# Kernel optimization log

Measured on AMD Instinct MI355X. Metric: run time of the kernel, lower is better.

Reference implementation:

```python
import jax, jax.numpy as jnp
import numpy as np

N_MB = 4  # number of micro-behavior buckets; C = N_MB**2 + 1

def setup_inputs() -> dict:
    key = jax.random.key(0)
    k_q, k_k, k_b, k_w, k_a = jax.random.split(key, 5)
    b, h, S, d = 8, 8, 512, 64
    C = N_MB * N_MB + 1
    return {
        "query": jax.random.normal(k_q, (b, h, S, d), dtype=jnp.float32),
        "key": jax.random.normal(k_k, (b, h, S, d), dtype=jnp.float32),
        "b_seq": jax.random.randint(k_b, (b, S), 0, N_MB + 1, dtype=jnp.int32),
        "W1": jax.random.normal(k_w, (N_MB, h, d, d), dtype=jnp.float32) * 0.02,
        "alpha1": jax.random.normal(k_a, (C, N_MB, h), dtype=jnp.float32) * 0.02,
    }

def reference(query, key, b_seq, W1, alpha1):
    # bucket-pair index per (i, j) token pair; 0 if either token is padding
    bi = b_seq[:, :, None]  # [b, S, 1]
    bj = b_seq[:, None, :]  # [b, 1, S]
    b_mat = ((bi - 1) * N_MB + bj) * (bi * bj != 0).astype(jnp.int32)  # [b, S, S]
    # mix the n_mb base bilinear weights into C per-bucket-pair matrices
    W1_ = jnp.einsum('Bhmn,CBh->Chmn', W1, jax.nn.softmax(alpha1, axis=1))
    # full bilinear score for every bucket-pair class C (the wasteful part)
    att_all = jnp.einsum('bhim,Chmn,bhjn->bhijC', query, W1_, key)  # [b,h,S,S,C]
    # select the score matching each pair's bucket index
    idx = b_mat[:, None, :, :, None].astype(jnp.int32)  # [b,1,S,S,1] -> broadcast over h
    idx = jnp.broadcast_to(idx, att_all.shape[:4] + (1,))
    scores = jnp.take_along_axis(att_all, idx, axis=4)[..., 0]  # [b,h,S,S]
    return scores
```

## Files before the change

### kernel.cpp

```cpp
#include <hip/hip_runtime.h>
#include <stdint.h>

#define NB 4
#define NC 17
#define HH 8
#define SS 512
#define DD 64
#define CT 64

typedef __attribute__((ext_vector_type(8))) short bf16x8;
typedef __attribute__((ext_vector_type(4))) float f32x4;

#define WS_W1   0
#define WS_RIDX 1114112
#define WS_GST  (WS_RIDX + 16384)

__device__ __forceinline__ unsigned short f2bf(float f) {
  unsigned int x; __builtin_memcpy(&x, &f, 4);
  return (unsigned short)((x + 0x7fff + ((x >> 16) & 1)) >> 16);
}
__device__ __forceinline__ bf16x8 cvt8(float4 a, float4 b) {
  union { bf16x8 v; unsigned short u[8]; } t;
  t.u[0] = f2bf(a.x); t.u[1] = f2bf(a.y); t.u[2] = f2bf(a.z); t.u[3] = f2bf(a.w);
  t.u[4] = f2bf(b.x); t.u[5] = f2bf(b.y); t.u[6] = f2bf(b.z); t.u[7] = f2bf(b.w);
  return t.v;
}

__global__ __launch_bounds__(256) void k_prep(const int* __restrict__ bseq,
                                              const float* __restrict__ W1,
                                              const float* __restrict__ alpha,
                                              int* __restrict__ ridx,
                                              int* __restrict__ gst,
                                              unsigned short* __restrict__ W1mbf) {
  int tid = threadIdx.x;
  if (blockIdx.x < 8) {
    int b = blockIdx.x;
    __shared__ int cnt[5], base[6], cur[5];
    if (tid < 5) cnt[tid] = 0;
    __syncthreads();
    for (int j = tid; j < SS; j += blockDim.x) atomicAdd(&cnt[bseq[b * SS + j]], 1);
    __syncthreads();
    if (tid == 0) {
      base[0] = 0;
      for (int k = 0; k < 5; k++) base[k + 1] = base[k] + cnt[k];
      for (int k = 0; k < 6; k++) gst[b * 6 + k] = base[k];
    }
    __syncthreads();
    if (tid < 5) cur[tid] = base[tid];
    __syncthreads();
    for (int j = tid; j < SS; j += blockDim.x) {
      int p = atomicAdd(&cur[bseq[b * SS + j]], 1);
      ridx[b * SS + p] = j;
    }
  } else {
    int cb = blockIdx.x - 8;
    int c = cb >> 3, hh = cb & 7;
    __shared__ float sm[NB];
    if (tid == 0) {
      float a[NB], mx = -1e30f;
      for (int B = 0; B < NB; B++) { a[B] = alpha[(c * NB + B) * HH + hh]; mx = fmaxf(mx, a[B]); }
      float s = 0.f;
      for (int B = 0; B < NB; B++) { a[B] = __expf(a[B] - mx); s += a[B]; }
      for (int B = 0; B < NB; B++) sm[B] = a[B] / s;
    }
    __syncthreads();
    float s0 = sm[0], s1 = sm[1], s2 = sm[2], s3 = sm[3];
    const float* w0p = &W1[((0 * HH + hh) << 12)];
    const float* w1p = &W1[((1 * HH + hh) << 12)];
    const float* w2p = &W1[((2 * HH + hh) << 12)];
    const float* w3p = &W1[((3 * HH + hh) << 12)];
    unsigned short* dst = &W1mbf[((size_t)(c * HH + hh)) << 12];
    for (int idx = tid * 4; idx < DD * DD; idx += 1024) {
      float4 w0 = *(const float4*)(w0p + idx);
      float4 w1 = *(const float4*)(w1p + idx);
      float4 w2 = *(const float4*)(w2p + idx);
      float4 w3 = *(const float4*)(w3p + idx);
      union { unsigned short u[4]; uint2 v; } o;
      o.u[0] = f2bf(w0.x * s0 + w1.x * s1 + w2.x * s2 + w3.x * s3);
      o.u[1] = f2bf(w0.y * s0 + w1.y * s1 + w2.y * s2 + w3.y * s3);
      o.u[2] = f2bf(w0.z * s0 + w1.z * s1 + w2.z * s2 + w3.z * s3);
      o.u[3] = f2bf(w0.w * s0 + w1.w * s1 + w2.w * s2 + w3.w * s3);
      *(uint2*)(dst + idx) = o.v;
    }
  }
}

__global__ __launch_bounds__(768, 6) void k_fused(const float* __restrict__ query,
                                                  const float* __restrict__ key,
                                                  const int* __restrict__ bseq,
                                                  const unsigned short* __restrict__ W1mbf,
                                                  const int* __restrict__ ridx,
                                                  const int* __restrict__ gst,
                                                  float* __restrict__ out) {
  int bx = blockIdx.x;
  int bh = bx & 63, jt = bx >> 6;
  int b = bh >> 3, h = bh & 7;
  int j0 = jt * CT;
  int tid = threadIdx.x, wave = tid >> 6, lane = tid & 63;
  int quad = lane >> 4, l16 = lane & 15;

  __shared__ __align__(16) unsigned short Tl[5][CT][72];
  __shared__ int ord[CT];
  __shared__ int ridxs[SS];
  __shared__ int p1list[40], p2list[40];
  __shared__ int n1tot, n2tot;

  if (tid < SS) ridxs[tid] = ridx[b * SS + tid];

  if (wave == 0) {
    int mybj = bseq[b * SS + j0 + lane];
    unsigned long long mm[5];
    int pb[6];
    pb[0] = 0;
#pragma unroll
    for (int a = 0; a < 5; a++) {
      mm[a] = __ballot(mybj == a);
      pb[a + 1] = pb[a] + (int)__popcll(mm[a]);
    }
    int pos = pb[mybj] + (int)__popcll(mm[mybj] & ((1ull << lane) - 1ull));
    ord[pos] = lane;

    int n1b_[5]; int t = 0;
#pragma unroll
    for (int a = 0; a < 5; a++) {
      n1b_[a] = t;
      t += ((pb[a + 1] - pb[a] + 15) >> 4) * ((a == 0) ? 1 : 5);
    }
    if (lane == 0) n1tot = t;

    if (lane < 5) {
      int a = lane;
      int ls = pb[a], le = pb[a + 1];
      int w = n1b_[a];
      for (int t0 = ls; t0 < le; t0 += 16) {
        if (a == 0) {
          p1list[w++] = t0 | (le << 6) | (1 << 21);
        } else {
#pragma unroll
          for (int B = 0; B < 5; B++) {
            int c = (B == 0) ? 0 : (B - 1) * NB + a;
            p1list[w++] = t0 | (le << 6) | (c << 13) | (B << 18);
          }
        }
      }
      int g[6];
#pragma unroll
      for (int k = 0; k < 6; k++) g[k] = gst[b * 6 + k];
      int w2 = 0;
      for (int aa = 0; aa < a; aa++) w2 += (g[aa + 1] - g[aa] + 15) >> 4;
      int gs = g[a], ge = g[a + 1];
      for (int p0 = gs; p0 < ge; p0 += 16)
        p2list[w2++] = p0 | (ge << 10) | (a << 20);
      if (a == 4) n2tot = w2;
    }
  }
  __syncthreads();

  for (int idx = wave; idx < n1tot; idx += 12) {
    int e = p1list[idx];
    int t0 = e & 63, le = (e >> 6) & 127, c = (e >> 13) & 31, B = (e >> 18) & 7;
    int bc = (e >> 21) & 1;
    const unsigned short* Wc = W1mbf + ((size_t)(c * HH + h) << 12);
    int p = t0 + l16; if (p > le - 1) p = le - 1;
    int cl = ord[p];
    const float* kp = &key[((size_t)(bh * SS + j0 + cl)) * DD + quad * 8];
    float4 ka = *(const float4*)kp, kb = *(const float4*)(kp + 4);
    float4 kc = *(const float4*)(kp + 32), kd = *(const float4*)(kp + 36);
    bf16x8 af0 = cvt8(ka, kb);
    bf16x8 af1 = cvt8(kc, kd);
    int cr[4];
#pragma unroll
    for (int reg = 0; reg < 4; reg++) {
      int pr = t0 + quad * 4 + reg;
      cr[reg] = (pr < le) ? ord[pr] : -1;
    }
    f32x4 acc[4];
#pragma unroll
    for (int nt = 0; nt < 4; nt++) {
      const unsigned short* wp = &Wc[(l16 * 4 + nt) * DD + quad * 8];
      bf16x8 b0 = *(const bf16x8*)wp;
      bf16x8 b1 = *(const bf16x8*)(wp + 32);
      f32x4 z = {0.f, 0.f, 0.f, 0.f};
      __builtin_amdgcn_s_setprio(1);
      z = __builtin_amdgcn_mfma_f32_16x16x32_bf16(af0, b0, z, 0, 0, 0);
      z = __builtin_amdgcn_mfma_f32_16x16x32_bf16(af1, b1, z, 0, 0, 0);
      __builtin_amdgcn_s_setprio(0);
      acc[nt] = z;
    }
#pragma unroll
    for (int reg = 0; reg < 4; reg++) {
      if (cr[reg] >= 0) {
        union { unsigned short u[4]; uint2 v; } o;
        o.u[0] = f2bf(acc[0][reg]); o.u[1] = f2bf(acc[1][reg]);
        o.u[2] = f2bf(acc[2][reg]); o.u[3] = f2bf(acc[3][reg]);
        if (bc) {
#pragma unroll
          for (int Bw = 0; Bw < 5; Bw++) *(uint2*)&Tl[Bw][cr[reg]][l16 * 4] = o.v;
        } else {
          *(uint2*)&Tl[B][cr[reg]][l16 * 4] = o.v;
        }
      }
    }
  }
  __syncthreads();

  for (int i0 = wave * 2; i0 < n2tot; i0 += 24) {
    int e0 = p2list[i0];
    bool has1 = (i0 + 1) < n2tot;
    int e1 = has1 ? p2list[i0 + 1] : e0;

    int p0a = e0 & 1023, gea = (e0 >> 10) & 1023, Ba = e0 >> 20;
    int p0b = e1 & 1023, geb = (e1 >> 10) & 1023, Bb = e1 >> 20;

    int pa = p0a + l16; if (pa > gea - 1) pa = gea - 1;
    int ra = ridxs[pa];
    const float* qa = &query[((size_t)(bh * SS + ra)) * DD + quad * 8];
    float4 a0 = *(const float4*)qa, a1 = *(const float4*)(qa + 4);
    float4 a2 = *(const float4*)(qa + 32), a3 = *(const float4*)(qa + 36);
    bf16x8 afa0 = cvt8(a0, a1), afa1 = cvt8(a2, a3);

    int pb_ = p0b + l16; if (pb_ > geb - 1) pb_ = geb - 1;
    int rb = ridxs[pb_];
    const float* qb = &query[((size_t)(bh * SS + rb)) * DD + quad * 8];
    float4 b0_ = *(const float4*)qb, b1_ = *(const float4*)(qb + 4);
    float4 b2_ = *(const float4*)(qb + 32), b3_ = *(const float4*)(qb + 36);
    bf16x8 afb0 = cvt8(b0_, b1_), afb1 = cvt8(b2_, b3_);

    int rra[4], rrb[4];
#pragma unroll
    for (int reg = 0; reg < 4; reg++) {
      int pra = p0a + quad * 4 + reg;
      rra[reg] = (pra < gea) ? ridxs[pra] : -1;
      int prb = p0b + quad * 4 + reg;
      rrb[reg] = (has1 && prb < geb) ? ridxs[prb] : -1;
    }

    f32x4 acca[4], accb[4];
#pragma unroll
    for (int ct = 0; ct < 4; ct++) {
      const unsigned short* tpa = &Tl[Ba][l16 * 4 + ct][quad * 8];
      const unsigned short* tpb = &Tl[Bb][l16 * 4 + ct][quad * 8];
      bf16x8 ba0 = *(const bf16x8*)tpa;
      bf16x8 ba1 = *(const bf16x8*)(tpa + 32);
      bf16x8 bb0 = *(const bf16x8*)tpb;
      bf16x8 bb1 = *(const bf16x8*)(tpb + 32);
      f32x4 za = {0.f, 0.f, 0.f, 0.f}, zb = {0.f, 0.f, 0.f, 0.f};
      __builtin_amdgcn_s_setprio(1);
      za = __builtin_amdgcn_mfma_f32_16x16x32_bf16(afa0, ba0, za, 0, 0, 0);
      zb = __builtin_amdgcn_mfma_f32_16x16x32_bf16(afb0, bb0, zb, 0, 0, 0);
      za = __builtin_amdgcn_mfma_f32_16x16x32_bf16(afa1, ba1, za, 0, 0, 0);
      zb = __builtin_amdgcn_mfma_f32_16x16x32_bf16(afb1, bb1, zb, 0, 0, 0);
      __builtin_amdgcn_s_setprio(0);
      acca[ct] = za; accb[ct] = zb;
    }
#pragma unroll
    for (int reg = 0; reg < 4; reg++) {
      if (rra[reg] >= 0) {
        f32x4 v = {acca[0][reg], acca[1][reg], acca[2][reg], acca[3][reg]};
        *(f32x4*)&out[((size_t)(bh * SS + rra[reg])) * SS + j0 + l16 * 4] = v;
      }
      if (rrb[reg] >= 0) {
        f32x4 v = {accb[0][reg], accb[1][reg], accb[2][reg], accb[3][reg]};
        *(f32x4*)&out[((size_t)(bh * SS + rrb[reg])) * SS + j0 + l16 * 4] = v;
      }
    }
  }
}

extern "C" void kernel_launch(void* const* d_in, const int* in_sizes, int n_in,
                              void* d_out, int out_size, void* d_ws, size_t ws_size,
                              hipStream_t stream) {
  const float* q = (const float*)d_in[0];
  const float* k = (const float*)d_in[1];
  const int* bseq = (const int*)d_in[2];
  const float* W1 = (const float*)d_in[3];
  const float* alpha = (const float*)d_in[4];
  float* out = (float*)d_out;
  char* ws = (char*)d_ws;
  unsigned short* W1mbf = (unsigned short*)(ws + WS_W1);
  int* ridx = (int*)(ws + WS_RIDX);
  int* gst = (int*)(ws + WS_GST);

  hipLaunchKernelGGL(k_prep, dim3(8 + NC * HH), dim3(256), 0, stream,
                     bseq, W1, alpha, ridx, gst, W1mbf);
  hipLaunchKernelGGL(k_fused, dim3(64 * (SS / CT)), dim3(768), 0, stream,
                     q, k, bseq, W1mbf, ridx, gst, out);
}
```

Baseline: 116.2 us.

## Add 128-column tile fused kernel with swizzled dynamic LDS and fallback

Adds a variant of the fused kernel that processes 128 key columns per block instead of 64. The per-bucket transformed key tiles live in XOR-swizzled dynamic shared memory, and each wave computes two query groups at once, writing 8-float vectors. The aim is to reuse each gathered query row across twice as many columns and to halve the number of blocks, which cuts redundant query loads and per-block setup. In exchange it uses more LDS per block and lowers occupancy to 3 blocks, and it falls back to the old 64-column kernel if the shared memory attribute cannot be set.

```diff
diff --git a/kernel.cpp b/kernel.cpp
--- a/kernel.cpp
+++ b/kernel.cpp
@@ -6,10 +6,10 @@
 #define HH 8
 #define SS 512
 #define DD 64
-#define CT 64
 
 typedef __attribute__((ext_vector_type(8))) short bf16x8;
 typedef __attribute__((ext_vector_type(4))) float f32x4;
+typedef __attribute__((ext_vector_type(8))) float f32x8;
 
 #define WS_W1   0
 #define WS_RIDX 1114112
@@ -85,22 +85,215 @@
   }
 }
 
-__global__ __launch_bounds__(768, 6) void k_fused(const float* __restrict__ query,
-                                                  const float* __restrict__ key,
-                                                  const int* __restrict__ bseq,
-                                                  const unsigned short* __restrict__ W1mbf,
-                                                  const int* __restrict__ ridx,
-                                                  const int* __restrict__ gst,
-                                                  float* __restrict__ out) {
+__global__ __launch_bounds__(768, 3) void k_fused128(const float* __restrict__ query,
+                                                     const float* __restrict__ key,
+                                                     const int* __restrict__ bseq,
+                                                     const unsigned short* __restrict__ W1mbf,
+                                                     const int* __restrict__ ridx,
+                                                     const int* __restrict__ gst,
+                                                     float* __restrict__ out) {
   int bx = blockIdx.x;
   int bh = bx & 63, jt = bx >> 6;
   int b = bh >> 3, h = bh & 7;
-  int j0 = jt * CT;
+  int j0 = jt * 128;
   int tid = threadIdx.x, wave = tid >> 6, lane = tid & 63;
   int quad = lane >> 4, l16 = lane & 15;
 
-  __shared__ __align__(16) unsigned short Tl[5][CT][72];
-  __shared__ int ord[CT];
+  extern __shared__ __align__(16) char dynls[];
+  __shared__ int ord[128];
+  __shared__ int ridxs[SS];
+  __shared__ int p1list[64], p2list[40];
+  __shared__ int n1tot, n2tot;
+
+#define TLP128(Bp, rowp, colByte) \
+  ((unsigned short*)(dynls + (((Bp) * 128 + (rowp)) << 7) + \
+                     ((colByte) ^ ((((rowp) >> 3) & 7) << 4))))
+
+  if (tid < SS) ridxs[tid] = ridx[b * SS + tid];
+
+  if (wave == 0) {
+    int c0 = bseq[b * SS + j0 + lane];
+    int c1 = bseq[b * SS + j0 + 64 + lane];
+    unsigned long long m0[5], m1[5];
+    int pb[6];
+    pb[0] = 0;
+#pragma unroll
+    for (int a = 0; a < 5; a++) {
+      m0[a] = __ballot(c0 == a);
+      m1[a] = __ballot(c1 == a);
+      pb[a + 1] = pb[a] + (int)__popcll(m0[a]) + (int)__popcll(m1[a]);
+    }
+    unsigned long long below = (1ull << lane) - 1ull;
+    int pos0 = pb[c0] + (int)__popcll(m0[c0] & below);
+    ord[pos0] = lane;
+    int pos1 = pb[c1] + (int)__popcll(m0[c1]) + (int)__popcll(m1[c1] & below);
+    ord[pos1] = 64 + lane;
+
+    int n1b_[5]; int t = 0;
+#pragma unroll
+    for (int a = 0; a < 5; a++) {
+      n1b_[a] = t;
+      t += ((pb[a + 1] - pb[a] + 15) >> 4) * ((a == 0) ? 1 : 5);
+    }
+    if (lane == 0) n1tot = t;
+
+    if (lane < 5) {
+      int a = lane;
+      int ls = pb[a], le = pb[a + 1];
+      int w = n1b_[a];
+      for (int t0 = ls; t0 < le; t0 += 16) {
+        if (a == 0) {
+          p1list[w++] = t0 | (le << 7) | (1 << 23);
+        } else {
+#pragma unroll
+          for (int B = 0; B < 5; B++) {
+            int c = (B == 0) ? 0 : (B - 1) * NB + a;
+            p1list[w++] = t0 | (le << 7) | (c << 15) | (B << 20);
+          }
+        }
+      }
+      int g[6];
+#pragma unroll
+      for (int k = 0; k < 6; k++) g[k] = gst[b * 6 + k];
+      int w2 = 0;
+      for (int aa = 0; aa < a; aa++) w2 += (g[aa + 1] - g[aa] + 15) >> 4;
+      int gs = g[a], ge = g[a + 1];
+      for (int p0 = gs; p0 < ge; p0 += 16)
+        p2list[w2++] = p0 | (ge << 10) | (a << 20);
+      if (a == 4) n2tot = w2;
+    }
+  }
+  __syncthreads();
+
+  for (int idx = wave; idx < n1tot; idx += 12) {
+    int e = p1list[idx];
+    int t0 = e & 127, le = (e >> 7) & 255, c = (e >> 15) & 31, B = (e >> 20) & 7;
+    int bc = (e >> 23) & 1;
+    const unsigned short* Wc = W1mbf + ((size_t)(c * HH + h) << 12);
+    int p = t0 + l16; if (p > le - 1) p = le - 1;
+    int cl = ord[p];
+    const float* kp = &key[((size_t)(bh * SS + j0 + cl)) * DD + quad * 8];
+    float4 ka = *(const float4*)kp, kb = *(const float4*)(kp + 4);
+    float4 kc = *(const float4*)(kp + 32), kd = *(const float4*)(kp + 36);
+    bf16x8 af0 = cvt8(ka, kb);
+    bf16x8 af1 = cvt8(kc, kd);
+    int cr[4];
+#pragma unroll
+    for (int reg = 0; reg < 4; reg++) {
+      int pr = t0 + quad * 4 + reg;
+      cr[reg] = (pr < le) ? ord[pr] : -1;
+    }
+    f32x4 acc[4];
+#pragma unroll
+    for (int nt = 0; nt < 4; nt++) {
+      const unsigned short* wp = &Wc[(l16 * 4 + nt) * DD + quad * 8];
+      bf16x8 b0 = *(const bf16x8*)wp;
+      bf16x8 b1 = *(const bf16x8*)(wp + 32);
+      f32x4 z = {0.f, 0.f, 0.f, 0.f};
+      __builtin_amdgcn_s_setprio(1);
+      z = __builtin_amdgcn_mfma_f32_16x16x32_bf16(af0, b0, z, 0, 0, 0);
+      z = __builtin_amdgcn_mfma_f32_16x16x32_bf16(af1, b1, z, 0, 0, 0);
+      __builtin_amdgcn_s_setprio(0);
+      acc[nt] = z;
+    }
+#pragma unroll
+    for (int reg = 0; reg < 4; reg++) {
+      if (cr[reg] >= 0) {
+        union { unsigned short u[4]; uint2 v; } o;
+        o.u[0] = f2bf(acc[0][reg]); o.u[1] = f2bf(acc[1][reg]);
+        o.u[2] = f2bf(acc[2][reg]); o.u[3] = f2bf(acc[3][reg]);
+        if (bc) {
+#pragma unroll
+          for (int Bw = 0; Bw < 5; Bw++) *(uint2*)TLP128(Bw, cr[reg], l16 * 8) = o.v;
+        } else {
+          *(uint2*)TLP128(B, cr[reg], l16 * 8) = o.v;
+        }
+      }
+    }
+  }
+  __syncthreads();
+
+  for (int i0 = wave * 2; i0 < n2tot; i0 += 24) {
+    int e0 = p2list[i0];
+    bool has1 = (i0 + 1) < n2tot;
+    int e1 = has1 ? p2list[i0 + 1] : e0;
+
+    int p0a = e0 & 1023, gea = (e0 >> 10) & 1023, Ba = e0 >> 20;
+    int p0b = e1 & 1023, geb = (e1 >> 10) & 1023, Bb = e1 >> 20;
+
+    int pa = p0a + l16; if (pa > gea - 1) pa = gea - 1;
+    int ra = ridxs[pa];
+    const float* qa = &query[((size_t)(bh * SS + ra)) * DD + quad * 8];
+    float4 a0 = *(const float4*)qa, a1 = *(const float4*)(qa + 4);
+    float4 a2 = *(const float4*)(qa + 32), a3 = *(const float4*)(qa + 36);
+    bf16x8 afa0 = cvt8(a0, a1), afa1 = cvt8(a2, a3);
+
+    int pb_ = p0b + l16; if (pb_ > geb - 1) pb_ = geb - 1;
+    int rb = ridxs[pb_];
+    const float* qb = &query[((size_t)(bh * SS + rb)) * DD + quad * 8];
+    float4 b0_ = *(const float4*)qb, b1_ = *(const float4*)(qb + 4);
+    float4 b2_ = *(const float4*)(qb + 32), b3_ = *(const float4*)(qb + 36);
+    bf16x8 afb0 = cvt8(b0_, b1_), afb1 = cvt8(b2_, b3_);
+
+    int rra[4], rrb[4];
+#pragma unroll
+    for (int reg = 0; reg < 4; reg++) {
+      int pra = p0a + quad * 4 + reg;
+      rra[reg] = (pra < gea) ? ridxs[pra] : -1;
+      int prb = p0b + quad * 4 + reg;
+      rrb[reg] = (has1 && prb < geb) ? ridxs[prb] : -1;
+    }
+
+    f32x4 acca[8], accb[8];
+#pragma unroll
+    for (int ct = 0; ct < 8; ct++) {
+      int rA = l16 * 8 + ct;
+      bf16x8 ba0 = *(const bf16x8*)TLP128(Ba, rA, quad * 16);
+      bf16x8 ba1 = *(const bf16x8*)TLP128(Ba, rA, 64 + quad * 16);
+      bf16x8 bb0 = *(const bf16x8*)TLP128(Bb, rA, quad * 16);
+      bf16x8 bb1 = *(const bf16x8*)TLP128(Bb, rA, 64 + quad * 16);
+      f32x4 za = {0.f, 0.f, 0.f, 0.f}, zb = {0.f, 0.f, 0.f, 0.f};
+      __builtin_amdgcn_s_setprio(1);
+      za = __builtin_amdgcn_mfma_f32_16x16x32_bf16(afa0, ba0, za, 0, 0, 0);
+      zb = __builtin_amdgcn_mfma_f32_16x16x32_bf16(afb0, bb0, zb, 0, 0, 0);
+      za = __builtin_amdgcn_mfma_f32_16x16x32_bf16(afa1, ba1, za, 0, 0, 0);
+      zb = __builtin_amdgcn_mfma_f32_16x16x32_bf16(afb1, bb1, zb, 0, 0, 0);
+      __builtin_amdgcn_s_setprio(0);
+      acca[ct] = za; accb[ct] = zb;
+    }
+#pragma unroll
+    for (int reg = 0; reg < 4; reg++) {
+      if (rra[reg] >= 0) {
+        f32x8 v = {acca[0][reg], acca[1][reg], acca[2][reg], acca[3][reg],
+                   acca[4][reg], acca[5][reg], acca[6][reg], acca[7][reg]};
+        *(f32x8*)&out[((size_t)(bh * SS + rra[reg])) * SS + j0 + l16 * 8] = v;
+      }
+      if (rrb[reg] >= 0) {
+        f32x8 v = {accb[0][reg], accb[1][reg], accb[2][reg], accb[3][reg],
+                   accb[4][reg], accb[5][reg], accb[6][reg], accb[7][reg]};
+        *(f32x8*)&out[((size_t)(bh * SS + rrb[reg])) * SS + j0 + l16 * 8] = v;
+      }
+    }
+  }
+#undef TLP128
+}
+
+__global__ __launch_bounds__(768, 6) void k_fused64(const float* __restrict__ query,
+                                                    const float* __restrict__ key,
+                                                    const int* __restrict__ bseq,
+                                                    const unsigned short* __restrict__ W1mbf,
+                                                    const int* __restrict__ ridx,
+                                                    const int* __restrict__ gst,
+                                                    float* __restrict__ out) {
+  int bx = blockIdx.x;
+  int bh = bx & 63, jt = bx >> 6;
+  int b = bh >> 3, h = bh & 7;
+  int j0 = jt * 64;
+  int tid = threadIdx.x, wave = tid >> 6, lane = tid & 63;
+  int quad = lane >> 4, l16 = lane & 15;
+
+  __shared__ __align__(16) unsigned short Tl[5][64][72];
+  __shared__ int ord[64];
   __shared__ int ridxs[SS];
   __shared__ int p1list[40], p2list[40];
   __shared__ int n1tot, n2tot;
@@ -283,6 +476,20 @@
 
   hipLaunchKernelGGL(k_prep, dim3(8 + NC * HH), dim3(256), 0, stream,
                      bseq, W1, alpha, ridx, gst, W1mbf);
-  hipLaunchKernelGGL(k_fused, dim3(64 * (SS / CT)), dim3(768), 0, stream,
-                     q, k, bseq, W1mbf, ridx, gst, out);
-}
+
+  static int use128 = -1;
+  if (use128 < 0) {
+    hipError_t e = hipFuncSetAttribute((const void*)k_fused128,
+                                       hipFuncAttributeMaxDynamicSharedMemorySize,
+                                       5 * 128 * 128);
+    use128 = (e == hipSuccess) ? 1 : 0;
+  }
+  if (use128) {
+    hipLaunchKernelGGL(k_fused128, dim3(64 * (SS / 128)), dim3(768),
+                       5 * 128 * 128, stream,
+                       q, k, bseq, W1mbf, ridx, gst, out);
+  } else {
+    hipLaunchKernelGGL(k_fused64, dim3(64 * (SS / 64)), dim3(768), 0, stream,
+                       q, k, bseq, W1mbf, ridx, gst, out);
+  }
+}
```

Measured after the change: 117.5 us. Within noise of the previous version (+1.2%).
